# Performance work log

Hardware: AMD Instinct MI355X
Metric: run time of the kernel (lower is better)

## Reference

```python
import jax, jax.numpy as jnp
import numpy as np
from jax import lax

NUM_HEADS = 1
DN = ('NCHW', 'OIHW', 'NCHW')
EPS = 1e-12  # F.normalize default eps


def _l2_normalize(t):
    # F.normalize(t, dim=-1): t / max(||t||_2, eps)
    n = jnp.sqrt(jnp.sum(t * t, axis=-1, keepdims=True))
    return t / jnp.maximum(n, EPS)


def setup_inputs() -> dict:
    key = jax.random.key(0)
    k0, k1, k2, k3 = jax.random.split(key, 4)
    b, c, h, w = 4, 48, 256, 256
    x = jax.random.normal(k0, (b, c, h, w), dtype=jnp.float32)
    qkv_w = jax.random.normal(k1, (3 * c, c, 1, 1), dtype=jnp.float32) * 0.05
    dw_w = jax.random.normal(k2, (3 * c, 1, 3, 3), dtype=jnp.float32) * 0.05
    proj_w = jax.random.normal(k3, (c, c, 1, 1), dtype=jnp.float32) * 0.05
    temperature = jnp.ones((NUM_HEADS, 1, 1), dtype=jnp.float32)
    return {"x": x, "qkv_w": qkv_w, "dw_w": dw_w, "proj_w": proj_w,
            "temperature": temperature}


def reference(x, qkv_w, dw_w, proj_w, temperature):
    b, c, h, w = x.shape
    heads = NUM_HEADS
    # 1x1 conv to 3c channels, then 3x3 depthwise conv (groups = 3c)
    qkv = lax.conv_general_dilated(x, qkv_w, (1, 1), 'VALID', dimension_numbers=DN)
    qkv = lax.conv_general_dilated(qkv, dw_w, (1, 1), ((1, 1), (1, 1)),
                                   feature_group_count=3 * c, dimension_numbers=DN)
    q, k, v = jnp.split(qkv, 3, axis=1)
    # [b, heads, c_per_head, h*w]
    q = q.reshape(b, heads, c // heads, h * w)
    k = k.reshape(b, heads, c // heads, h * w)
    v = v.reshape(b, heads, c // heads, h * w)
    q = _l2_normalize(q)
    k = _l2_normalize(k)
    # channel-wise attention: [b, heads, c_per_head, c_per_head]
    attn = jax.nn.softmax(jnp.einsum('bhcn,bhdn->bhcd', q, k) * temperature, axis=-1)
    out = jnp.einsum('bhcd,bhdn->bhcn', attn, v).reshape(b, c, h, w)
    return lax.conv_general_dilated(out, proj_w, (1, 1), 'VALID', dimension_numbers=DN)
```

## Files before the change

### kernel.cpp

```cpp
#include <hip/hip_runtime.h>

#define B 4
#define C 48
#define C3 144
#define H 256
#define W 256
#define HW 65536
#define EPSN 1e-12f

#define TSX 16
#define TSY 12
#define HSX 18
#define HSY 14
#define NTX 16
#define NTY 22
#define NPIX2 192
#define NHALO 252

#define NCHUNK 128
#define CHUNK 512
#define LP 68

#define S_QKV_OFF  ((size_t)0)
#define S_DWQ_OFF  (S_QKV_OFF + (size_t)B * C3 * HW)
#define S_DWK_OFF  (S_DWQ_OFF + (size_t)B * C * HW)
#define S_SP_OFF   (S_DWK_OFF + (size_t)B * C * HW)
#define S_NQP_OFF  (S_SP_OFF + (size_t)B * NCHUNK * C * C)
#define S_NKP_OFF  (S_NQP_OFF + (size_t)B * NCHUNK * C)
#define S_S_OFF    (S_NKP_OFF + (size_t)B * NCHUNK * C)
#define S_NQ_OFF   (S_S_OFF + (size_t)B * C * C)
#define S_NK_OFF   (S_NQ_OFF + (size_t)B * C)
#define S_M_OFF    (S_NK_OFF + (size_t)B * C)
#define S_WT_OFF   (S_M_OFF + (size_t)B * C * C)
#define S_FLOATS   (S_WT_OFF + (size_t)C3 * C)

#define A_DWQ_OFF  ((size_t)0)
#define A_DWK_OFF  (A_DWQ_OFF + (size_t)B * C * HW)
#define A_SP_OFF   (A_DWK_OFF + (size_t)B * C * HW)
#define A_NQP_OFF  (A_SP_OFF + (size_t)B * NCHUNK * C * C)
#define A_NKP_OFF  (A_NQP_OFF + (size_t)B * NCHUNK * C)
#define A_S_OFF    (A_NKP_OFF + (size_t)B * NCHUNK * C)
#define A_NQ_OFF   (A_S_OFF + (size_t)B * C * C)
#define A_NK_OFF   (A_NQ_OFF + (size_t)B * C)
#define A_M_OFF    (A_NK_OFF + (size_t)B * C)
#define A_FLOATS   (A_M_OFF + (size_t)B * C * C)

#define B_S_OFF  0
#define B_NQ_OFF (B * C * C)
#define B_NK_OFF (B_NQ_OFF + B * C)
#define B_M_OFF  (B_NK_OFF + B * C)
#define B_ZERO_N (B * C * C + 2 * B * C)


__global__ __launch_bounds__(256) void s_wt(
    const float* __restrict__ w1, float* __restrict__ wT) {
  const int i = blockIdx.x * 256 + threadIdx.x;
  if (i < C3 * C) {
    const int oc = i / C, d = i - oc * C;
    wT[d * C3 + oc] = w1[i];
  }
}

__global__ __launch_bounds__(256) void s_conv1x1(
    const float* __restrict__ x, const float* __restrict__ wT,
    float* __restrict__ qkv) {
  __shared__ float xs[C * 64];
  __shared__ float wsm[C * C3];
  const int t = threadIdx.x;
  const int bb = blockIdx.x >> 10;
  const int p0 = (blockIdx.x & 1023) << 6;
  const float* xb = x + (size_t)bb * C * HW + p0;
#pragma unroll
  for (int j = 0; j < 3; ++j) {
    const int f = t + j * 256;
    const int d = f >> 4, p4 = (f & 15) * 4;
    *(float4*)&xs[d * 64 + p4] = *(const float4*)&xb[(size_t)d * HW + p4];
  }
  for (int i = t; i < (C * C3) / 4; i += 256)
    ((float4*)wsm)[i] = ((const float4*)wT)[i];
  __syncthreads();
  const int pl = t & 63;
  const int oc0 = (t >> 6) * 36;
  float acc[36];
#pragma unroll
  for (int j = 0; j < 36; ++j) acc[j] = 0.f;
#pragma unroll 4
  for (int d = 0; d < C; ++d) {
    const float vd = xs[d * 64 + pl];
    const float* wrow = wsm + d * C3 + oc0;
#pragma unroll
    for (int jj = 0; jj < 9; ++jj) {
      const float4 wv = *(const float4*)&wrow[jj * 4];
      acc[jj * 4 + 0] = fmaf(wv.x, vd, acc[jj * 4 + 0]);
      acc[jj * 4 + 1] = fmaf(wv.y, vd, acc[jj * 4 + 1]);
      acc[jj * 4 + 2] = fmaf(wv.z, vd, acc[jj * 4 + 2]);
      acc[jj * 4 + 3] = fmaf(wv.w, vd, acc[jj * 4 + 3]);
    }
  }
  float* ob = qkv + ((size_t)bb * C3 + oc0) * HW + p0 + pl;
#pragma unroll
  for (int j = 0; j < 36; ++j) ob[(size_t)j * HW] = acc[j];
}

#define DWR 16
__global__ __launch_bounds__(256) void s_dw(
    const float* __restrict__ qkv, const float* __restrict__ w9,
    float* __restrict__ dwq, float* __restrict__ dwk,
    float* __restrict__ vout) {
  __shared__ float ls[18 * 260];
  const int t = threadIdx.x;
  const int rblk = blockIdx.x & 15;
  const int cb = blockIdx.x >> 4;
  const int c = cb % C3;
  const int bb = cb / C3;
  const int r0 = rblk * DWR;
  const float* src = qkv + (size_t)cb * HW;
#pragma unroll
  for (int f = t; f < 18 * 256; f += 256) {
    const int rr = f >> 8, xc = f & 255;
    const int gr = r0 - 1 + rr;
    ls[rr * 260 + 1 + xc] = (gr >= 0 && gr < H) ? src[gr * W + xc] : 0.f;
  }
  if (t < 18) { ls[t * 260] = 0.f; ls[t * 260 + 257] = 0.f; }
  const float* wp = w9 + c * 9;
  float wv[9];
#pragma unroll
  for (int k = 0; k < 9; ++k) wv[k] = wp[k];
  __syncthreads();
  float* dst;
  int cc;
  if (c < C)          { dst = dwq;  cc = c; }
  else if (c < 2 * C) { dst = dwk;  cc = c - C; }
  else                { dst = vout; cc = c - 2 * C; }
  float* ob = dst + ((size_t)bb * C + cc) * HW;
  const int xx = t;
#pragma unroll
  for (int ry = 0; ry < DWR; ++ry) {
    const float* l0 = ls + ry * 260 + xx;
    float d = wv[0] * l0[0] + wv[1] * l0[1] + wv[2] * l0[2];
    d = fmaf(wv[3], l0[260], d);
    d = fmaf(wv[4], l0[261], d);
    d = fmaf(wv[5], l0[262], d);
    d = fmaf(wv[6], l0[520], d);
    d = fmaf(wv[7], l0[521], d);
    d = fmaf(wv[8], l0[522], d);
    ob[(r0 + ry) * W + xx] = d;
  }
}


__global__ __launch_bounds__(256) void a1_conv_dw(
    const float* __restrict__ x, const float* __restrict__ w1,
    const float* __restrict__ w9, float* __restrict__ dwq,
    float* __restrict__ dwk, float* __restrict__ vout) {
  __shared__ float xs[C * 256];
  __shared__ float qs[8 * 256];
  __shared__ float wg[C * 8];
  __shared__ float wg9[8 * 9];
  const int t = threadIdx.x;
  const int bb = blockIdx.x / (NTX * NTY);
  const int tile = blockIdx.x % (NTX * NTY);
  const int ty = tile / NTX, tx = tile % NTX;

  const int hyy = t / HSX, hxx = t % HSX;
  const int hy = ty * TSY - 1 + hyy;
  const int hx = tx * TSX - 1 + hxx;
  const bool hin = (t < NHALO) && (hy >= 0) && (hy < H) && (hx >= 0) && (hx < W);
  const float* xb = x + (size_t)bb * C * HW + (hin ? (hy * W + hx) : 0);
#pragma unroll
  for (int ic = 0; ic < C; ++ic)
    xs[ic * 256 + t] = hin ? xb[(size_t)ic * HW] : 0.f;

  const int py = t / TSX, px = t % TSX;
  const int gy = ty * TSY + py, gx = tx * TSX + px;
  const bool pin = (t < NPIX2) && (gy < H);
  const int hpos = py * HSX + px;

  for (int grp = 0; grp < 18; ++grp) {
    const int ch0 = grp * 8;
    {
      const int j = t + ((t < 128) ? 256 : 0);
      if (t < 128) {
        const int ic = t >> 3, g = t & 7;
        wg[t] = w1[(ch0 + g) * C + ic];
        const int ic2 = j >> 3, g2 = j & 7;
        wg[j] = w1[(ch0 + g2) * C + ic2];
      } else if (t < 256) {
        const int r = t - 128;
        const int ic = (r + 128) >> 3, g = (r + 128) & 7;
        wg[r + 128] = w1[(ch0 + g) * C + ic];
      }
      if (t < 72) wg9[t] = w9[ch0 * 9 + t];
    }
    __syncthreads();

    float a[8];
#pragma unroll
    for (int g = 0; g < 8; ++g) a[g] = 0.f;
#pragma unroll 4
    for (int ic = 0; ic < C; ++ic) {
      const float xsv = xs[ic * 256 + t];
      const float4 w0 = *(const float4*)&wg[ic * 8];
      const float4 w4 = *(const float4*)&wg[ic * 8 + 4];
      a[0] = fmaf(w0.x, xsv, a[0]);
      a[1] = fmaf(w0.y, xsv, a[1]);
      a[2] = fmaf(w0.z, xsv, a[2]);
      a[3] = fmaf(w0.w, xsv, a[3]);
      a[4] = fmaf(w4.x, xsv, a[4]);
      a[5] = fmaf(w4.y, xsv, a[5]);
      a[6] = fmaf(w4.z, xsv, a[6]);
      a[7] = fmaf(w4.w, xsv, a[7]);
    }
#pragma unroll
    for (int g = 0; g < 8; ++g) qs[g * 256 + t] = a[g];
    __syncthreads();
    if (t < NPIX2) {
#pragma unroll
      for (int g = 0; g < 8; ++g) {
        const int ch = ch0 + g;
        const float* w9p = wg9 + g * 9;
        const float* q = qs + g * 256 + hpos;
        float d = w9p[0] * q[0] + w9p[1] * q[1] + w9p[2] * q[2];
        d = fmaf(w9p[3], q[HSX], d);
        d = fmaf(w9p[4], q[HSX + 1], d);
        d = fmaf(w9p[5], q[HSX + 2], d);
        d = fmaf(w9p[6], q[2 * HSX], d);
        d = fmaf(w9p[7], q[2 * HSX + 1], d);
        d = fmaf(w9p[8], q[2 * HSX + 2], d);
        if (pin) {
          float* dst;
          int cc;
          if (ch < C)          { dst = dwq; cc = ch; }
          else if (ch < 2 * C) { dst = dwk; cc = ch - C; }
          else                 { dst = vout; cc = ch - 2 * C; }
          dst[((size_t)bb * C + cc) * HW + gy * W + gx] = d;
        }
      }
    }
    __syncthreads();
  }
}

__global__ __launch_bounds__(256) void a2_gram(
    const float* __restrict__ dwq, const float* __restrict__ dwk,
    float* __restrict__ Sp, float* __restrict__ nqp, float* __restrict__ nkp) {
  __shared__ float qs[C * LP];
  __shared__ float ks[C * LP];
  const int tid = threadIdx.x;
  const int bb = blockIdx.x / NCHUNK;
  const int chunk = blockIdx.x % NCHUNK;
  const int base = chunk * CHUNK;
  const float* qb = dwq + (size_t)bb * C * HW + base;
  const float* kb = dwk + (size_t)bb * C * HW + base;
  const int c0 = (tid >> 4) * 3;
  const int d0 = (tid & 15) * 3;
  float acc[3][3] = {{0.f}};
  float nacc = 0.f;
  for (int sub = 0; sub < CHUNK / 64; ++sub) {
    __syncthreads();
#pragma unroll
    for (int j = 0; j < 3; ++j) {
      const int f = tid + j * 256;
      const int cc = f >> 4, p4 = (f & 15) * 4;
      *(float4*)&qs[cc * LP + p4] = *(const float4*)&qb[(size_t)cc * HW + sub * 64 + p4];
      *(float4*)&ks[cc * LP + p4] = *(const float4*)&kb[(size_t)cc * HW + sub * 64 + p4];
    }
    __syncthreads();
    if (tid < C) {
#pragma unroll
      for (int pp = 0; pp < 64; ++pp) { const float v = qs[tid * LP + pp]; nacc = fmaf(v, v, nacc); }
    } else if (tid >= 64 && tid < 64 + C) {
      const int c = tid - 64;
#pragma unroll
      for (int pp = 0; pp < 64; ++pp) { const float v = ks[c * LP + pp]; nacc = fmaf(v, v, nacc); }
    }
#pragma unroll 8
    for (int pp = 0; pp < 64; ++pp) {
      const float q0 = qs[(c0 + 0) * LP + pp];
      const float q1 = qs[(c0 + 1) * LP + pp];
      const float q2 = qs[(c0 + 2) * LP + pp];
      const float k0 = ks[(d0 + 0) * LP + pp];
      const float k1 = ks[(d0 + 1) * LP + pp];
      const float k2 = ks[(d0 + 2) * LP + pp];
      acc[0][0] = fmaf(q0, k0, acc[0][0]);
      acc[0][1] = fmaf(q0, k1, acc[0][1]);
      acc[0][2] = fmaf(q0, k2, acc[0][2]);
      acc[1][0] = fmaf(q1, k0, acc[1][0]);
      acc[1][1] = fmaf(q1, k1, acc[1][1]);
      acc[1][2] = fmaf(q1, k2, acc[1][2]);
      acc[2][0] = fmaf(q2, k0, acc[2][0]);
      acc[2][1] = fmaf(q2, k1, acc[2][1]);
      acc[2][2] = fmaf(q2, k2, acc[2][2]);
    }
  }
  float* Sb = Sp + ((size_t)bb * NCHUNK + chunk) * C * C;
#pragma unroll
  for (int i = 0; i < 3; ++i)
#pragma unroll
    for (int j = 0; j < 3; ++j)
      Sb[(c0 + i) * C + (d0 + j)] = acc[i][j];
  if (tid < C)                        nqp[((size_t)bb * NCHUNK + chunk) * C + tid] = nacc;
  else if (tid >= 64 && tid < 64 + C) nkp[((size_t)bb * NCHUNK + chunk) * C + (tid - 64)] = nacc;
}

#define RED_N (B * C * C + 2 * B * C)
__global__ __launch_bounds__(256) void a3a_reduce(
    const float* __restrict__ Sp, const float* __restrict__ nqp,
    const float* __restrict__ nkp, float* __restrict__ S,
    float* __restrict__ nq, float* __restrict__ nk) {
  const int gid = blockIdx.x * 256 + threadIdx.x;
  if (gid < B * C * C) {
    const int bb = gid / (C * C), j = gid - bb * (C * C);
    const float* src = Sp + (size_t)bb * NCHUNK * C * C + j;
    float s = 0.f;
#pragma unroll 8
    for (int i = 0; i < NCHUNK; ++i) s += src[(size_t)i * C * C];
    S[gid] = s;
  } else if (gid < B * C * C + B * C) {
    const int r = gid - B * C * C;
    const int bb = r / C, j = r - bb * C;
    const float* src = nqp + (size_t)bb * NCHUNK * C + j;
    float s = 0.f;
#pragma unroll 8
    for (int i = 0; i < NCHUNK; ++i) s += src[(size_t)i * C];
    nq[r] = s;
  } else if (gid < RED_N) {
    const int r = gid - B * C * C - B * C;
    const int bb = r / C, j = r - bb * C;
    const float* src = nkp + (size_t)bb * NCHUNK * C + j;
    float s = 0.f;
#pragma unroll 8
    for (int i = 0; i < NCHUNK; ++i) s += src[(size_t)i * C];
    nk[r] = s;
  }
}

__global__ __launch_bounds__(64) void a3b_attn(
    const float* __restrict__ S, const float* __restrict__ nq,
    const float* __restrict__ nk, const float* __restrict__ proj_w,
    const float* __restrict__ temperature, float* __restrict__ M) {
  __shared__ float A[C * C];
  __shared__ float knl[C];
  const int bb = blockIdx.x;
  const int t = threadIdx.x;
  const float T = temperature[0];
  if (t < C) knl[t] = fmaxf(sqrtf(nk[bb * C + t]), EPSN);
  __syncthreads();
  if (t < C) {
    const float qn = fmaxf(sqrtf(nq[bb * C + t]), EPSN);
    float row[C];
    float m = -1e30f;
    for (int d = 0; d < C; ++d) {
      const float v = S[(size_t)bb * C * C + t * C + d] / (qn * knl[d]) * T;
      row[d] = v;
      m = fmaxf(m, v);
    }
    float sum = 0.f;
    for (int d = 0; d < C; ++d) { const float e = expf(row[d] - m); row[d] = e; sum += e; }
    const float inv = 1.f / sum;
    for (int d = 0; d < C; ++d) A[t * C + d] = row[d] * inv;
  }
  __syncthreads();
  for (int idx = t; idx < C * C; idx += 64) {
    const int e = idx / C, d = idx % C;
    float acc = 0.f;
    for (int cc = 0; cc < C; ++cc) acc = fmaf(proj_w[e * C + cc], A[cc * C + d], acc);
    M[(size_t)bb * C * C + idx] = acc;
  }
}

__global__ __launch_bounds__(256) void a4_apply(
    float* __restrict__ out, const float* __restrict__ M) {
  __shared__ float vs[C * 64];
  __shared__ float Ms[C * C];
  const int t = threadIdx.x;
  const int bb = blockIdx.x >> 10;
  const int p0 = (blockIdx.x & 1023) << 6;
  float* ob = out + (size_t)bb * C * HW + p0;
#pragma unroll
  for (int j = 0; j < 3; ++j) {
    const int f = t + j * 256;
    const int d = f >> 4, p4 = (f & 15) * 4;
    *(float4*)&vs[d * 64 + p4] = *(const float4*)&ob[(size_t)d * HW + p4];
  }
  for (int j = t; j < C * C; j += 256) Ms[j] = M[bb * C * C + j];
  __syncthreads();
  const int pl = t & 63;
  const int e0 = (t >> 6) * 12;
  float acc[12];
#pragma unroll
  for (int j = 0; j < 12; ++j) acc[j] = 0.f;
  for (int d = 0; d < C; ++d) {
    const float vd = vs[d * 64 + pl];
#pragma unroll
    for (int j = 0; j < 12; ++j) acc[j] = fmaf(Ms[(e0 + j) * C + d], vd, acc[j]);
  }
#pragma unroll
  for (int j = 0; j < 12; ++j) ob[(size_t)(e0 + j) * HW + pl] = acc[j];
}


__global__ __launch_bounds__(256) void k0_zero(float* __restrict__ ws) {
  const int i = blockIdx.x * 256 + threadIdx.x;
  if (i < B_ZERO_N) ws[i] = 0.f;
}

#define TS 14
#define HS 16
#define NT 19
#define NPIX 196

__global__ __launch_bounds__(256) void k1_fused(
    const float* __restrict__ x, const float* __restrict__ w1,
    const float* __restrict__ w9, float* __restrict__ vout,
    float* __restrict__ S, float* __restrict__ nq, float* __restrict__ nk) {
  __shared__ float qs[4 * 256];
  __shared__ float qt[NPIX * C];
  __shared__ float kt[NPIX * C];
  const int t = threadIdx.x;
  const int bb = blockIdx.x / (NT * NT);
  const int tile = blockIdx.x % (NT * NT);
  const int ty = tile / NT, tx = tile % NT;
  const int hy = ty * TS - 1 + (t >> 4);
  const int hx = tx * TS - 1 + (t & 15);
  const bool hin = (hy >= 0 && hy < H && hx >= 0 && hx < W);
  const float* xb = x + (size_t)bb * C * HW;
  float xv[C];
#pragma unroll
  for (int ic = 0; ic < C; ++ic)
    xv[ic] = hin ? xb[(size_t)ic * HW + hy * W + hx] : 0.f;
  const int py = t / TS, px = t % TS;
  const int gy = ty * TS + py, gx = tx * TS + px;
  const bool pin = (t < NPIX) && (gy < H) && (gx < W);
  for (int grp = 0; grp < 36; ++grp) {
    const int ch0 = grp * 4;
    const float* wp = w1 + ch0 * C;
    float a0 = 0.f, a1 = 0.f, a2 = 0.f, a3 = 0.f;
#pragma unroll
    for (int ic = 0; ic < C; ++ic) {
      const float xs = xv[ic];
      a0 = fmaf(wp[ic], xs, a0);
      a1 = fmaf(wp[C + ic], xs, a1);
      a2 = fmaf(wp[2 * C + ic], xs, a2);
      a3 = fmaf(wp[3 * C + ic], xs, a3);
    }
    qs[0 * 256 + t] = a0;
    qs[1 * 256 + t] = a1;
    qs[2 * 256 + t] = a2;
    qs[3 * 256 + t] = a3;
    __syncthreads();
    if (t < NPIX) {
#pragma unroll
      for (int g = 0; g < 4; ++g) {
        const int ch = ch0 + g;
        const float* w9p = w9 + ch * 9;
        const float* q = qs + g * 256 + py * HS + px;
        float d = w9p[0] * q[0] + w9p[1] * q[1] + w9p[2] * q[2];
        d = fmaf(w9p[3], q[HS], d);
        d = fmaf(w9p[4], q[HS + 1], d);
        d = fmaf(w9p[5], q[HS + 2], d);
        d = fmaf(w9p[6], q[2 * HS], d);
        d = fmaf(w9p[7], q[2 * HS + 1], d);
        d = fmaf(w9p[8], q[2 * HS + 2], d);
        if (ch < C)          qt[t * C + ch] = pin ? d : 0.f;
        else if (ch < 2 * C) kt[t * C + (ch - C)] = pin ? d : 0.f;
        else if (pin)        vout[((size_t)bb * C + (ch - 2 * C)) * HW + gy * W + gx] = d;
      }
    }
    __syncthreads();
  }
  if (t < C) {
    float s = 0.f;
    for (int p = 0; p < NPIX; ++p) { const float v = qt[p * C + t]; s = fmaf(v, v, s); }
    atomicAdd(&nq[bb * C + t], s);
  } else if (t >= 64 && t < 64 + C) {
    const int c = t - 64;
    float s = 0.f;
    for (int p = 0; p < NPIX; ++p) { const float v = kt[p * C + c]; s = fmaf(v, v, s); }
    atomicAdd(&nk[bb * C + c], s);
  }
  {
    const int part = t >> 6;
    const int idx = t & 63;
    const int c0 = (idx >> 3) * 6;
    const int d0 = (idx & 7) * 6;
    float acc[6][6] = {{0.f}};
    const int p0 = part * 49;
    for (int p = p0; p < p0 + 49; ++p) {
      float qv[6], kv[6];
#pragma unroll
      for (int j = 0; j < 6; ++j) { qv[j] = qt[p * C + c0 + j]; kv[j] = kt[p * C + d0 + j]; }
#pragma unroll
      for (int i = 0; i < 6; ++i)
#pragma unroll
        for (int j = 0; j < 6; ++j) acc[i][j] = fmaf(qv[i], kv[j], acc[i][j]);
    }
    float* Sb = S + (size_t)bb * C * C;
#pragma unroll
    for (int i = 0; i < 6; ++i)
#pragma unroll
      for (int j = 0; j < 6; ++j) atomicAdd(&Sb[(c0 + i) * C + (d0 + j)], acc[i][j]);
  }
}


extern "C" void kernel_launch(void* const* d_in, const int* in_sizes, int n_in,
                              void* d_out, int out_size, void* d_ws, size_t ws_size,
                              hipStream_t stream) {
  const float* x      = (const float*)d_in[0];
  const float* qkv_w  = (const float*)d_in[1];
  const float* dw_w   = (const float*)d_in[2];
  const float* proj_w = (const float*)d_in[3];
  const float* temp   = (const float*)d_in[4];
  float* out = (float*)d_out;
  float* ws  = (float*)d_ws;

  if (ws_size >= S_FLOATS * sizeof(float)) {
    float* qkv = ws + S_QKV_OFF;
    float* dwq = ws + S_DWQ_OFF;
    float* dwk = ws + S_DWK_OFF;
    float* Sp  = ws + S_SP_OFF;
    float* nqp = ws + S_NQP_OFF;
    float* nkp = ws + S_NKP_OFF;
    float* S   = ws + S_S_OFF;
    float* nq  = ws + S_NQ_OFF;
    float* nk  = ws + S_NK_OFF;
    float* M   = ws + S_M_OFF;
    float* wT  = ws + S_WT_OFF;
    s_wt<<<(C3 * C + 255) / 256, 256, 0, stream>>>(qkv_w, wT);
    s_conv1x1<<<B * 1024, 256, 0, stream>>>(x, wT, qkv);
    s_dw<<<B * C3 * 16, 256, 0, stream>>>(qkv, dw_w, dwq, dwk, out);
    a2_gram<<<B * NCHUNK, 256, 0, stream>>>(dwq, dwk, Sp, nqp, nkp);
    a3a_reduce<<<(RED_N + 255) / 256, 256, 0, stream>>>(Sp, nqp, nkp, S, nq, nk);
    a3b_attn<<<B, 64, 0, stream>>>(S, nq, nk, proj_w, temp, M);
    a4_apply<<<B * 1024, 256, 0, stream>>>(out, M);
  } else if (ws_size >= A_FLOATS * sizeof(float)) {
    float* dwq = ws + A_DWQ_OFF;
    float* dwk = ws + A_DWK_OFF;
    float* Sp  = ws + A_SP_OFF;
    float* nqp = ws + A_NQP_OFF;
    float* nkp = ws + A_NKP_OFF;
    float* S   = ws + A_S_OFF;
    float* nq  = ws + A_NQ_OFF;
    float* nk  = ws + A_NK_OFF;
    float* M   = ws + A_M_OFF;
    a1_conv_dw<<<B * NTX * NTY, 256, 0, stream>>>(x, qkv_w, dw_w, dwq, dwk, out);
    a2_gram<<<B * NCHUNK, 256, 0, stream>>>(dwq, dwk, Sp, nqp, nkp);
    a3a_reduce<<<(RED_N + 255) / 256, 256, 0, stream>>>(Sp, nqp, nkp, S, nq, nk);
    a3b_attn<<<B, 64, 0, stream>>>(S, nq, nk, proj_w, temp, M);
    a4_apply<<<B * 1024, 256, 0, stream>>>(out, M);
  } else {
    float* S  = ws + B_S_OFF;
    float* nq = ws + B_NQ_OFF;
    float* nk = ws + B_NK_OFF;
    float* M  = ws + B_M_OFF;
    k0_zero<<<(B_ZERO_N + 255) / 256, 0, 0, stream>>>(ws);
    k1_fused<<<B * NT * NT, 256, 0, stream>>>(x, qkv_w, dw_w, out, S, nq, nk);
    a3b_attn<<<B, 64, 0, stream>>>(S, nq, nk, proj_w, temp, M);
    a4_apply<<<B * 1024, 256, 0, stream>>>(out, M);
  }
}
```

Before: 351.2 us.

## Retile 1x1 conv to 4 pixels x 12 channels per thread with scalar weight loads

```diff
diff --git a/kernel.cpp b/kernel.cpp
--- a/kernel.cpp
+++ b/kernel.cpp
@@ -64,42 +64,52 @@
 __global__ __launch_bounds__(256) void s_conv1x1(
     const float* __restrict__ x, const float* __restrict__ wT,
     float* __restrict__ qkv) {
-  __shared__ float xs[C * 64];
-  __shared__ float wsm[C * C3];
+  __shared__ float xs[C * 256];
   const int t = threadIdx.x;
-  const int bb = blockIdx.x >> 10;
-  const int p0 = (blockIdx.x & 1023) << 6;
+  const int bb = blockIdx.x >> 8;
+  const int p0 = (blockIdx.x & 255) << 8;
   const float* xb = x + (size_t)bb * C * HW + p0;
 #pragma unroll
-  for (int j = 0; j < 3; ++j) {
+  for (int j = 0; j < 12; ++j) {
     const int f = t + j * 256;
-    const int d = f >> 4, p4 = (f & 15) * 4;
-    *(float4*)&xs[d * 64 + p4] = *(const float4*)&xb[(size_t)d * HW + p4];
-  }
-  for (int i = t; i < (C * C3) / 4; i += 256)
-    ((float4*)wsm)[i] = ((const float4*)wT)[i];
+    const int d = f >> 6, p4 = (f & 63) * 4;
+    *(float4*)&xs[d * 256 + p4] = *(const float4*)&xb[(size_t)d * HW + p4];
+  }
   __syncthreads();
-  const int pl = t & 63;
-  const int oc0 = (t >> 6) * 36;
-  float acc[36];
-#pragma unroll
-  for (int j = 0; j < 36; ++j) acc[j] = 0.f;
+  const int pl = (t & 63) * 4;
+  const int ocw = __builtin_amdgcn_readfirstlane((t >> 6) * 12);
+#pragma unroll 1
+  for (int g = 0; g < 3; ++g) {
+    const int oc0 = g * 48 + ocw;
+    const float* wp = wT + oc0;
+    float acc[12][4];
+#pragma unroll
+    for (int o = 0; o < 12; ++o)
+#pragma unroll
+      for (int p = 0; p < 4; ++p) acc[o][p] = 0.f;
 #pragma unroll 4
-  for (int d = 0; d < C; ++d) {
-    const float vd = xs[d * 64 + pl];
-    const float* wrow = wsm + d * C3 + oc0;
-#pragma unroll
-    for (int jj = 0; jj < 9; ++jj) {
-      const float4 wv = *(const float4*)&wrow[jj * 4];
-      acc[jj * 4 + 0] = fmaf(wv.x, vd, acc[jj * 4 + 0]);
-      acc[jj * 4 + 1] = fmaf(wv.y, vd, acc[jj * 4 + 1]);
-      acc[jj * 4 + 2] = fmaf(wv.z, vd, acc[jj * 4 + 2]);
-      acc[jj * 4 + 3] = fmaf(wv.w, vd, acc[jj * 4 + 3]);
-    }
-  }
-  float* ob = qkv + ((size_t)bb * C3 + oc0) * HW + p0 + pl;
-#pragma unroll
-  for (int j = 0; j < 36; ++j) ob[(size_t)j * HW] = acc[j];
+    for (int d = 0; d < C; ++d) {
+      const float4 xv = *(const float4*)&xs[d * 256 + pl];
+      const float xa[4] = {xv.x, xv.y, xv.z, xv.w};
+#pragma unroll
+      for (int jj = 0; jj < 3; ++jj) {
+        const float4 wv = *(const float4*)&wp[d * C3 + jj * 4];
+        const float wa[4] = {wv.x, wv.y, wv.z, wv.w};
+#pragma unroll
+        for (int o = 0; o < 4; ++o)
+#pragma unroll
+          for (int p = 0; p < 4; ++p)
+            acc[jj * 4 + o][p] = fmaf(wa[o], xa[p], acc[jj * 4 + o][p]);
+      }
+    }
+    float* ob = qkv + ((size_t)bb * C3 + oc0) * HW + p0 + pl;
+#pragma unroll
+    for (int o = 0; o < 12; ++o) {
+      float4 v;
+      v.x = acc[o][0]; v.y = acc[o][1]; v.z = acc[o][2]; v.w = acc[o][3];
+      *(float4*)&ob[(size_t)o * HW] = v;
+    }
+  }
 }
 
 #define DWR 16
@@ -528,7 +538,7 @@
     float* M   = ws + S_M_OFF;
     float* wT  = ws + S_WT_OFF;
     s_wt<<<(C3 * C + 255) / 256, 256, 0, stream>>>(qkv_w, wT);
-    s_conv1x1<<<B * 1024, 256, 0, stream>>>(x, wT, qkv);
+    s_conv1x1<<<B * 256, 256, 0, stream>>>(x, wT, qkv);
     s_dw<<<B * C3 * 16, 256, 0, stream>>>(qkv, dw_w, dwq, dwk, out);
     a2_gram<<<B * NCHUNK, 256, 0, stream>>>(dwq, dwk, Sp, nqp, nkp);
     a3a_reduce<<<(RED_N + 255) / 256, 256, 0, stream>>>(Sp, nqp, nkp, S, nq, nk);
@@ -554,7 +564,7 @@
     float* nq = ws + B_NQ_OFF;
     float* nk = ws + B_NK_OFF;
     float* M  = ws + B_M_OFF;
-    k0_zero<<<(B_ZERO_N + 255) / 256, 0, 0, stream>>>(ws);
+    k0_zero<<<(B_ZERO_N + 255) / 256, 256, 0, stream>>>(ws);
     k1_fused<<<B * NT * NT, 256, 0, stream>>>(x, qkv_w, dw_w, out, S, nq, nk);
     a3b_attn<<<B, 64, 0, stream>>>(S, nq, nk, proj_w, temp, M);
     a4_apply<<<B * 1024, 256, 0, stream>>>(out, M);
```

Measured after the change: 345.0 us. Within noise of the previous version (-1.8%).
